# Kernel optimization log

Hardware: AMD Instinct MI355X
Metric: run time of the kernel (lower is better)

Reference implementation:

```python
import jax, jax.numpy as jnp
import numpy as np

KLD_SCALE = 10.0


def setup_inputs() -> dict:
    key = jax.random.key(0)
    k1, k2 = jax.random.split(key)
    B, C, H, W = 16, 64, 64, 64
    K = 1024
    inputs = jax.random.normal(k1, (B, C, H, W), dtype=jnp.float32)
    codebook = jax.random.normal(k2, (K, C), dtype=jnp.float32) * (1.0 / K)
    beta = jnp.float32(0.25)
    return {"inputs": inputs, "codebook": codebook, "beta": beta}


def reference(inputs, codebook, beta):
    # inputs: [B, C, H, W], codebook: [K, D] with D == C
    sg = jax.lax.stop_gradient
    x = jnp.transpose(inputs, (0, 2, 3, 1))          # [B, H, W, D]
    D = x.shape[-1]
    flat = x.reshape(-1, D)                           # [N, D]
    d = (jnp.sum(flat * flat, axis=1, keepdims=True)
         + jnp.sum(codebook * codebook, axis=1)
         - 2.0 * flat @ codebook.T)                   # [N, K]
    idx = jnp.argmin(d, axis=1)                       # [N]
    q = codebook[idx].reshape(x.shape)                # gather == one_hot @ codebook
    # training (non-EMA) loss: (beta*||q - sg(x)||^2 + ||sg(q) - x||^2) * kld_scale
    loss = beta * jnp.mean((q - sg(x)) ** 2)
    loss = (loss + jnp.mean((sg(q) - x) ** 2)) * KLD_SCALE
    # straight-through estimator
    q_st = x + sg(q - x)
    # perplexity from code usage histogram (== mean of one-hot rows)
    K = codebook.shape[0]
    counts = jnp.zeros((K,), dtype=flat.dtype).at[idx].add(1.0)
    e_mean = counts / flat.shape[0]
    perplexity = jnp.exp(-jnp.sum(e_mean * jnp.log(e_mean + 1e-10)))
    quantized = jnp.transpose(q_st, (0, 3, 1, 2))     # [B, C, H, W]
    return loss, quantized, perplexity
```

## Files before the change

kernel.cpp:

```cpp
#include <hip/hip_runtime.h>
#include <cfloat>

typedef __bf16 bf16x8 __attribute__((ext_vector_type(8)));
typedef float f32x16 __attribute__((ext_vector_type(16)));

namespace {
constexpr int kHW = 4096;
constexpr int kC = 64;
constexpr float kInvN = 1.0f / 65536.0f;


__global__ __launch_bounds__(256) void prep_kernel(
    const float* __restrict__ cb, uint4* __restrict__ frags,
    unsigned int* __restrict__ hist, float* __restrict__ lossacc) {
  const int c = blockIdx.x;
  const int t = threadIdx.x;
  const int lane = t & 63, wv = t >> 6;
  const int lo = lane & 31, hi = lane >> 5;
  const int code = c * 32 + lo;
  const int ks = wv;

  const float* row = cb + code * kC + ks * 16 + hi * 8;
  float4 v0 = *reinterpret_cast<const float4*>(row);
  float4 v1 = *reinterpret_cast<const float4*>(row + 4);
  float vv[8] = {v0.x, v0.y, v0.z, v0.w, v1.x, v1.y, v1.z, v1.w};
  bf16x8 fh, fl;
  #pragma unroll
  for (int e = 0; e < 8; ++e) {
    float v = -2.0f * vv[e];
    __bf16 h = (__bf16)v;
    fh[e] = h;
    fl[e] = (__bf16)(v - (float)h);
  }
  frags[(c * 9 + ks) * 64 + lane] = *reinterpret_cast<uint4*>(&fh);
  frags[(c * 9 + 4 + ks) * 64 + lane] = *reinterpret_cast<uint4*>(&fl);

  if (wv == 0) {
    bf16x8 fb;
    #pragma unroll
    for (int e = 0; e < 8; ++e) fb[e] = (__bf16)0.0f;
    if (hi == 0) {
      float s = 0.0f;
      #pragma unroll
      for (int d = 0; d < kC; d += 4) {
        float4 v = *reinterpret_cast<const float4*>(cb + code * kC + d);
        s = fmaf(v.x, v.x, fmaf(v.y, v.y, fmaf(v.z, v.z, fmaf(v.w, v.w, s))));
      }
      __bf16 h = (__bf16)s;
      fb[0] = h;
      fb[1] = (__bf16)(s - (float)h);
    }
    frags[(c * 9 + 8) * 64 + lane] = *reinterpret_cast<uint4*>(&fb);
  }
  if (t < 32) hist[c * 32 + t] = 0u;
  if (c == 0 && t == 0) lossacc[0] = 0.0f;
}

__global__ __launch_bounds__(256) void vq_argmin_kernel(
    const float* __restrict__ in, const bf16x8* __restrict__ frags,
    unsigned int* __restrict__ hist, unsigned int* __restrict__ idxOut) {
  __shared__ float sVal[4][32];
  __shared__ int sIdxW[4][32];
  const int t = threadIdx.x;
  const int lane = t & 63, wv = t >> 6;
  const int lo = lane & 31, hi = lane >> 5;
  const int sg2 = wv & 1, kh = wv >> 1;
  const int site = blockIdx.x * 64 + sg2 * 32 + lo;
  const int b = site >> 12, hw = site & 4095;
  const float* xp = in + b * (kC * kHW) + hw;

  bf16x8 Bh[4], Bl[4];
  #pragma unroll
  for (int ks = 0; ks < 4; ++ks) {
    #pragma unroll
    for (int e = 0; e < 8; ++e) {
      const int d = ks * 16 + hi * 8 + e;
      float v = xp[d * kHW];
      __bf16 h = (__bf16)v;
      Bh[ks][e] = h;
      Bl[ks][e] = (__bf16)(v - (float)h);
    }
  }
  bf16x8 ones;
  #pragma unroll
  for (int e = 0; e < 8; ++e) ones[e] = (__bf16)0.0f;
  if (hi == 0) { ones[0] = (__bf16)1.0f; ones[1] = (__bf16)1.0f; }
  f32x16 zero;
  #pragma unroll
  for (int r = 0; r < 16; ++r) zero[r] = 0.0f;

  float best[16];
  int bch[16];
  #pragma unroll
  for (int r = 0; r < 16; ++r) { best[r] = FLT_MAX; bch[r] = 0; }

  const bf16x8* fA = frags + lane;

  bf16x8 A0[9], A1[9];
  auto prefetch = [&](bf16x8(&F)[9], int c) {
    #pragma unroll
    for (int j = 0; j < 9; ++j) F[j] = fA[(c * 9 + j) * 64];
  };
  auto compute = [&](const bf16x8(&F)[9], int c) {
    f32x16 a = __builtin_amdgcn_mfma_f32_32x32x16_bf16(F[8], ones, zero, 0, 0, 0);
    #pragma unroll
    for (int ks = 0; ks < 4; ++ks)
      a = __builtin_amdgcn_mfma_f32_32x32x16_bf16(F[ks], Bh[ks], a, 0, 0, 0);
    #pragma unroll
    for (int ks = 0; ks < 4; ++ks)
      a = __builtin_amdgcn_mfma_f32_32x32x16_bf16(F[4 + ks], Bh[ks], a, 0, 0, 0);
    #pragma unroll
    for (int ks = 0; ks < 4; ++ks)
      a = __builtin_amdgcn_mfma_f32_32x32x16_bf16(F[ks], Bl[ks], a, 0, 0, 0);
    #pragma unroll
    for (int r = 0; r < 16; ++r) {
      bool p = a[r] < best[r];
      best[r] = p ? a[r] : best[r];
      bch[r] = p ? c : bch[r];
    }
  };

  const int c0 = kh * 16;
  prefetch(A0, c0);
  #pragma unroll 1
  for (int c = c0; c < c0 + 16; c += 2) {
    prefetch(A1, c + 1);
    compute(A0, c);
    if (c + 2 < c0 + 16) prefetch(A0, c + 2);
    compute(A1, c + 1);
  }

  float bv = best[0];
  int bidx = bch[0] * 32 + (hi << 2);
  #pragma unroll
  for (int r = 1; r < 16; ++r) {
    const int kloc = (r & 3) + 8 * (r >> 2) + (hi << 2);
    int idx = bch[r] * 32 + kloc;
    float v = best[r];
    if (v < bv || (v == bv && idx < bidx)) { bv = v; bidx = idx; }
  }
  float ov = __shfl_xor(bv, 32, 64);
  int oi = __shfl_xor(bidx, 32, 64);
  if (ov < bv || (ov == bv && oi < bidx)) { bv = ov; bidx = oi; }
  if (hi == 0) {
    sVal[wv][lo] = bv;
    sIdxW[wv][lo] = bidx;
  }
  __syncthreads();
  if (wv < 2 && hi == 0) {
    float v2 = sVal[wv + 2][lo];
    int i2 = sIdxW[wv + 2][lo];
    if (v2 < bv || (v2 == bv && i2 < bidx)) { bv = v2; bidx = i2; }
    idxOut[site] = (unsigned int)bidx;
    atomicAdd(&hist[bidx], 1u);
  }
}

__global__ __launch_bounds__(256) void epilogue_kernel(
    const float* __restrict__ in, const float* __restrict__ cb,
    const unsigned int* __restrict__ idx, float* __restrict__ lossacc,
    float* __restrict__ qout) {
  __shared__ float sRed[4];
  const int t = threadIdx.x;
  const int sg = t & 63, dg = t >> 6;
  const int siteBase = blockIdx.x * 256 + sg * 4;
  const int b = siteBase >> 12, hw = siteBase & 4095;
  const float* xb = in + b * (kC * kHW) + hw;
  float* ob = qout + b * (kC * kHW) + hw;
  uint4 cc = *reinterpret_cast<const uint4*>(idx + siteBase);
  const float* q0 = cb + cc.x * kC;
  const float* q1 = cb + cc.y * kC;
  const float* q2 = cb + cc.z * kC;
  const float* q3 = cb + cc.w * kC;
  float ls = 0.0f;
  #pragma unroll
  for (int j = 0; j < 16; ++j) {
    const int d = dg * 16 + j;
    float4 xv = *reinterpret_cast<const float4*>(xb + d * kHW);
    float d0 = q0[d] - xv.x;
    float d1 = q1[d] - xv.y;
    float d2 = q2[d] - xv.z;
    float d3 = q3[d] - xv.w;
    ls = fmaf(d0, d0, ls);
    ls = fmaf(d1, d1, ls);
    ls = fmaf(d2, d2, ls);
    ls = fmaf(d3, d3, ls);
    float* o = ob + d * kHW;
    o[0] = xv.x + d0;
    o[1] = xv.y + d1;
    o[2] = xv.z + d2;
    o[3] = xv.w + d3;
  }
  #pragma unroll
  for (int off = 32; off; off >>= 1) ls += __shfl_xor(ls, off, 64);
  if ((t & 63) == 0) sRed[t >> 6] = ls;
  __syncthreads();
  if (t == 0) {
    float s = (sRed[0] + sRed[1]) + (sRed[2] + sRed[3]);
    atomicAdd(lossacc, s);
  }
}

__global__ __launch_bounds__(1024) void finalize_kernel(
    const unsigned int* __restrict__ hist, const float* __restrict__ lossacc,
    const float* __restrict__ beta, float* __restrict__ out) {
  __shared__ float red[16];
  const int t = threadIdx.x;
  float e = (float)hist[t] * kInvN;
  float term = e * logf(e + 1e-10f);
  #pragma unroll
  for (int off = 32; off; off >>= 1) term += __shfl_xor(term, off, 64);
  if ((t & 63) == 0) red[t >> 6] = term;
  __syncthreads();
  if (t == 0) {
    float h = 0.0f;
    #pragma unroll
    for (int i = 0; i < 16; ++i) h += red[i];
    out[1 + 4194304] = expf(-h);
    out[0] = lossacc[0] * (1.0f + beta[0]) * 10.0f / 4194304.0f;
  }
}
}

extern "C" void kernel_launch(void* const* d_in, const int* in_sizes, int n_in,
                              void* d_out, int out_size, void* d_ws, size_t ws_size,
                              hipStream_t stream) {
  const float* inputs = (const float*)d_in[0];
  const float* cb = (const float*)d_in[1];
  const float* beta = (const float*)d_in[2];
  float* out = (float*)d_out;

  uint4* frags = (uint4*)d_ws;
  unsigned int* hist = (unsigned int*)((char*)d_ws + 294912);
  float* lossacc = (float*)((char*)d_ws + 299008);
  unsigned int* idx = (unsigned int*)((char*)d_ws + 299024);

  prep_kernel<<<32, 256, 0, stream>>>(cb, frags, hist, lossacc);
  vq_argmin_kernel<<<1024, 256, 0, stream>>>(inputs, (const bf16x8*)frags,
                                             hist, idx);
  epilogue_kernel<<<256, 256, 0, stream>>>(inputs, cb, idx, lossacc, out + 1);
  finalize_kernel<<<1, 1024, 0, stream>>>(hist, lossacc, beta, out);
}
```

Baseline: 121.2 us.

## Split codebook across four waves, each handling all 64 sites

Each wave now processes both 32-site groups of the block against one quarter of the codebook, instead of half the codebook for one site group. Every loaded codebook fragment feeds two independent MFMA chains, so each wave reads half as many fragment bytes per MFMA and has two accumulators to interleave and hide latency. The cost is roughly doubled register use for inputs, accumulators and best values, which may lower occupancy. The final reduction now merges four partial results per site in one wave.

After: 124.3 us. +2.5%, slower.

```diff
diff --git a/kernel.cpp b/kernel.cpp
--- a/kernel.cpp
+++ b/kernel.cpp
@@ -59,26 +59,31 @@
 __global__ __launch_bounds__(256) void vq_argmin_kernel(
     const float* __restrict__ in, const bf16x8* __restrict__ frags,
     unsigned int* __restrict__ hist, unsigned int* __restrict__ idxOut) {
-  __shared__ float sVal[4][32];
-  __shared__ int sIdxW[4][32];
+  __shared__ float sVal[4][64];
+  __shared__ int sIdxW[4][64];
   const int t = threadIdx.x;
   const int lane = t & 63, wv = t >> 6;
   const int lo = lane & 31, hi = lane >> 5;
-  const int sg2 = wv & 1, kh = wv >> 1;
-  const int site = blockIdx.x * 64 + sg2 * 32 + lo;
-  const int b = site >> 12, hw = site & 4095;
-  const float* xp = in + b * (kC * kHW) + hw;
-
-  bf16x8 Bh[4], Bl[4];
+  const int siteBase = blockIdx.x * 64;
+  const int b = siteBase >> 12;
+  const int hw0 = siteBase & 4095;
+  const float* xp0 = in + b * (kC * kHW) + hw0 + lo;
+  const float* xp1 = in + b * (kC * kHW) + hw0 + 32 + lo;
+
+  bf16x8 B0h[4], B0l[4], B1h[4], B1l[4];
   #pragma unroll
   for (int ks = 0; ks < 4; ++ks) {
     #pragma unroll
     for (int e = 0; e < 8; ++e) {
       const int d = ks * 16 + hi * 8 + e;
-      float v = xp[d * kHW];
-      __bf16 h = (__bf16)v;
-      Bh[ks][e] = h;
-      Bl[ks][e] = (__bf16)(v - (float)h);
+      float v0 = xp0[d * kHW];
+      __bf16 h0 = (__bf16)v0;
+      B0h[ks][e] = h0;
+      B0l[ks][e] = (__bf16)(v0 - (float)h0);
+      float v1 = xp1[d * kHW];
+      __bf16 h1 = (__bf16)v1;
+      B1h[ks][e] = h1;
+      B1l[ks][e] = (__bf16)(v1 - (float)h1);
     }
   }
   bf16x8 ones;
@@ -89,10 +94,13 @@
   #pragma unroll
   for (int r = 0; r < 16; ++r) zero[r] = 0.0f;
 
-  float best[16];
-  int bch[16];
-  #pragma unroll
-  for (int r = 0; r < 16; ++r) { best[r] = FLT_MAX; bch[r] = 0; }
+  float best0[16], best1[16];
+  int bch0[16], bch1[16];
+  #pragma unroll
+  for (int r = 0; r < 16; ++r) {
+    best0[r] = FLT_MAX; bch0[r] = 0;
+    best1[r] = FLT_MAX; bch1[r] = 0;
+  }
 
   const bf16x8* fA = frags + lane;
 
@@ -102,57 +110,81 @@
     for (int j = 0; j < 9; ++j) F[j] = fA[(c * 9 + j) * 64];
   };
   auto compute = [&](const bf16x8(&F)[9], int c) {
-    f32x16 a = __builtin_amdgcn_mfma_f32_32x32x16_bf16(F[8], ones, zero, 0, 0, 0);
-    #pragma unroll
-    for (int ks = 0; ks < 4; ++ks)
-      a = __builtin_amdgcn_mfma_f32_32x32x16_bf16(F[ks], Bh[ks], a, 0, 0, 0);
-    #pragma unroll
-    for (int ks = 0; ks < 4; ++ks)
-      a = __builtin_amdgcn_mfma_f32_32x32x16_bf16(F[4 + ks], Bh[ks], a, 0, 0, 0);
-    #pragma unroll
-    for (int ks = 0; ks < 4; ++ks)
-      a = __builtin_amdgcn_mfma_f32_32x32x16_bf16(F[ks], Bl[ks], a, 0, 0, 0);
+    f32x16 a0 = __builtin_amdgcn_mfma_f32_32x32x16_bf16(F[8], ones, zero, 0, 0, 0);
+    f32x16 a1 = __builtin_amdgcn_mfma_f32_32x32x16_bf16(F[8], ones, zero, 0, 0, 0);
+    #pragma unroll
+    for (int ks = 0; ks < 4; ++ks) {
+      a0 = __builtin_amdgcn_mfma_f32_32x32x16_bf16(F[ks], B0h[ks], a0, 0, 0, 0);
+      a1 = __builtin_amdgcn_mfma_f32_32x32x16_bf16(F[ks], B1h[ks], a1, 0, 0, 0);
+    }
+    #pragma unroll
+    for (int ks = 0; ks < 4; ++ks) {
+      a0 = __builtin_amdgcn_mfma_f32_32x32x16_bf16(F[4 + ks], B0h[ks], a0, 0, 0, 0);
+      a1 = __builtin_amdgcn_mfma_f32_32x32x16_bf16(F[4 + ks], B1h[ks], a1, 0, 0, 0);
+    }
+    #pragma unroll
+    for (int ks = 0; ks < 4; ++ks) {
+      a0 = __builtin_amdgcn_mfma_f32_32x32x16_bf16(F[ks], B0l[ks], a0, 0, 0, 0);
+      a1 = __builtin_amdgcn_mfma_f32_32x32x16_bf16(F[ks], B1l[ks], a1, 0, 0, 0);
+    }
     #pragma unroll
     for (int r = 0; r < 16; ++r) {
-      bool p = a[r] < best[r];
-      best[r] = p ? a[r] : best[r];
-      bch[r] = p ? c : bch[r];
+      bool p0 = a0[r] < best0[r];
+      best0[r] = p0 ? a0[r] : best0[r];
+      bch0[r] = p0 ? c : bch0[r];
+      bool p1 = a1[r] < best1[r];
+      best1[r] = p1 ? a1[r] : best1[r];
+      bch1[r] = p1 ? c : bch1[r];
     }
   };
 
-  const int c0 = kh * 16;
+  const int c0 = wv * 8;
   prefetch(A0, c0);
   #pragma unroll 1
-  for (int c = c0; c < c0 + 16; c += 2) {
+  for (int c = c0; c < c0 + 8; c += 2) {
     prefetch(A1, c + 1);
     compute(A0, c);
-    if (c + 2 < c0 + 16) prefetch(A0, c + 2);
+    if (c + 2 < c0 + 8) prefetch(A0, c + 2);
     compute(A1, c + 1);
   }
 
-  float bv = best[0];
-  int bidx = bch[0] * 32 + (hi << 2);
+  float bv0 = best0[0], bv1 = best1[0];
+  int bi0 = bch0[0] * 32 + (hi << 2);
+  int bi1 = bch1[0] * 32 + (hi << 2);
   #pragma unroll
   for (int r = 1; r < 16; ++r) {
     const int kloc = (r & 3) + 8 * (r >> 2) + (hi << 2);
-    int idx = bch[r] * 32 + kloc;
-    float v = best[r];
-    if (v < bv || (v == bv && idx < bidx)) { bv = v; bidx = idx; }
-  }
-  float ov = __shfl_xor(bv, 32, 64);
-  int oi = __shfl_xor(bidx, 32, 64);
-  if (ov < bv || (ov == bv && oi < bidx)) { bv = ov; bidx = oi; }
+    int i0 = bch0[r] * 32 + kloc;
+    float v0 = best0[r];
+    if (v0 < bv0 || (v0 == bv0 && i0 < bi0)) { bv0 = v0; bi0 = i0; }
+    int i1 = bch1[r] * 32 + kloc;
+    float v1 = best1[r];
+    if (v1 < bv1 || (v1 == bv1 && i1 < bi1)) { bv1 = v1; bi1 = i1; }
+  }
+  {
+    float ov = __shfl_xor(bv0, 32, 64);
+    int oi = __shfl_xor(bi0, 32, 64);
+    if (ov < bv0 || (ov == bv0 && oi < bi0)) { bv0 = ov; bi0 = oi; }
+    ov = __shfl_xor(bv1, 32, 64);
+    oi = __shfl_xor(bi1, 32, 64);
+    if (ov < bv1 || (ov == bv1 && oi < bi1)) { bv1 = ov; bi1 = oi; }
+  }
   if (hi == 0) {
-    sVal[wv][lo] = bv;
-    sIdxW[wv][lo] = bidx;
+    sVal[wv][lo] = bv0;       sIdxW[wv][lo] = bi0;
+    sVal[wv][32 + lo] = bv1;  sIdxW[wv][32 + lo] = bi1;
   }
   __syncthreads();
-  if (wv < 2 && hi == 0) {
-    float v2 = sVal[wv + 2][lo];
-    int i2 = sIdxW[wv + 2][lo];
-    if (v2 < bv || (v2 == bv && i2 < bidx)) { bv = v2; bidx = i2; }
-    idxOut[site] = (unsigned int)bidx;
-    atomicAdd(&hist[bidx], 1u);
+  if (wv == 0) {
+    float bb = sVal[0][lane];
+    int bi = sIdxW[0][lane];
+    #pragma unroll
+    for (int w2 = 1; w2 < 4; ++w2) {
+      float v2 = sVal[w2][lane];
+      int i2 = sIdxW[w2][lane];
+      if (v2 < bb || (v2 == bb && i2 < bi)) { bb = v2; bi = i2; }
+    }
+    idxOut[siteBase + lane] = (unsigned int)bi;
+    atomicAdd(&hist[bi], 1u);
   }
 }
 
```

## Stage input tile through LDS with vector loads and fully unroll codebook loop

Applied to the files above, without the earlier changes.

Each block now loads its 64x64 input tile into shared memory using coalesced float4 global loads, and waves build their bf16 hi/lo fragments from LDS. Before, each lane issued strided scalar global loads, and each input element was fetched twice, once by each codebook-half wave. The manual double-buffered prefetch of codebook fragments is replaced by a fully unrolled 16-iteration loop, leaving load scheduling to the compiler. This adds 16KB of LDS per block and a barrier, and the full unroll may raise register pressure and lower occupancy.

After: 138.6 us. 1.14x slower.

```diff
diff --git a/kernel.cpp b/kernel.cpp
--- a/kernel.cpp
+++ b/kernel.cpp
@@ -59,26 +59,40 @@
 __global__ __launch_bounds__(256) void vq_argmin_kernel(
     const float* __restrict__ in, const bf16x8* __restrict__ frags,
     unsigned int* __restrict__ hist, unsigned int* __restrict__ idxOut) {
+  __shared__ __align__(16) float sX[64][64];
   __shared__ float sVal[4][32];
   __shared__ int sIdxW[4][32];
   const int t = threadIdx.x;
   const int lane = t & 63, wv = t >> 6;
   const int lo = lane & 31, hi = lane >> 5;
-  const int sg2 = wv & 1, kh = wv >> 1;
-  const int site = blockIdx.x * 64 + sg2 * 32 + lo;
-  const int b = site >> 12, hw = site & 4095;
-  const float* xp = in + b * (kC * kHW) + hw;
+  const int g = wv & 1, h = wv >> 1;
+  const int siteBase = blockIdx.x * 64;
+  const int b = siteBase >> 12, hw0 = siteBase & 4095;
+  const float* xin = in + b * (kC * kHW) + hw0;
+
+  {
+    const int s4 = (t & 15) * 4;
+    const int d0 = t >> 4;
+    #pragma unroll
+    for (int i = 0; i < 4; ++i) {
+      const int d = d0 + i * 16;
+      *reinterpret_cast<float4*>(&sX[d][s4]) =
+          *reinterpret_cast<const float4*>(xin + d * kHW + s4);
+    }
+  }
+  __syncthreads();
 
   bf16x8 Bh[4], Bl[4];
+  const int col = g * 32 + lo;
   #pragma unroll
   for (int ks = 0; ks < 4; ++ks) {
     #pragma unroll
     for (int e = 0; e < 8; ++e) {
       const int d = ks * 16 + hi * 8 + e;
-      float v = xp[d * kHW];
-      __bf16 h = (__bf16)v;
-      Bh[ks][e] = h;
-      Bl[ks][e] = (__bf16)(v - (float)h);
+      float v = sX[d][col];
+      __bf16 hh = (__bf16)v;
+      Bh[ks][e] = hh;
+      Bl[ks][e] = (__bf16)(v - (float)hh);
     }
   }
   bf16x8 ones;
@@ -95,13 +109,14 @@
   for (int r = 0; r < 16; ++r) { best[r] = FLT_MAX; bch[r] = 0; }
 
   const bf16x8* fA = frags + lane;
-
-  bf16x8 A0[9], A1[9];
-  auto prefetch = [&](bf16x8(&F)[9], int c) {
+  const int c0 = h * 16;
+
+  #pragma unroll
+  for (int cc = 0; cc < 16; ++cc) {
+    const int c = c0 + cc;
+    bf16x8 F[9];
     #pragma unroll
     for (int j = 0; j < 9; ++j) F[j] = fA[(c * 9 + j) * 64];
-  };
-  auto compute = [&](const bf16x8(&F)[9], int c) {
     f32x16 a = __builtin_amdgcn_mfma_f32_32x32x16_bf16(F[8], ones, zero, 0, 0, 0);
     #pragma unroll
     for (int ks = 0; ks < 4; ++ks)
@@ -118,16 +133,6 @@
       best[r] = p ? a[r] : best[r];
       bch[r] = p ? c : bch[r];
     }
-  };
-
-  const int c0 = kh * 16;
-  prefetch(A0, c0);
-  #pragma unroll 1
-  for (int c = c0; c < c0 + 16; c += 2) {
-    prefetch(A1, c + 1);
-    compute(A0, c);
-    if (c + 2 < c0 + 16) prefetch(A0, c + 2);
-    compute(A1, c + 1);
   }
 
   float bv = best[0];
@@ -151,7 +156,7 @@
     float v2 = sVal[wv + 2][lo];
     int i2 = sIdxW[wv + 2][lo];
     if (v2 < bv || (v2 == bv && i2 < bidx)) { bv = v2; bidx = i2; }
-    idxOut[site] = (unsigned int)bidx;
+    idxOut[siteBase + g * 32 + lo] = (unsigned int)bidx;
     atomicAdd(&hist[bidx], 1u);
   }
 }
```

## Stage codebook fragments in LDS and give each wave all codes for its sites

Applied to the files above, without the earlier changes.

The argmin kernel now uses 512-thread blocks, each covering 256 sites. Each wave scans the full codebook for its own 32 sites, so the cross-wave LDS reduction goes away. Codebook fragments are copied into a 147KB LDS buffer in two halves with global_load_lds, instead of every wave reading them from global/L2. The MFMA chain is split into two independent accumulators to shorten dependency chains. Risks: the large LDS footprint allows only one block per CU, the 256-block grid is small, and the staging is serialized with no overlap between halves.

New measurement: 124.6 us. 2.8% more time.

```diff
diff --git a/kernel.cpp b/kernel.cpp
--- a/kernel.cpp
+++ b/kernel.cpp
@@ -8,6 +8,8 @@
 constexpr int kHW = 4096;
 constexpr int kC = 64;
 constexpr float kInvN = 1.0f / 65536.0f;
+constexpr int kChunkBytes = 9216;
+constexpr int kHalfBytes = 16 * kChunkBytes;
 
 
 __global__ __launch_bounds__(256) void prep_kernel(
@@ -56,18 +58,28 @@
   if (c == 0 && t == 0) lossacc[0] = 0.0f;
 }
 
-__global__ __launch_bounds__(256) void vq_argmin_kernel(
-    const float* __restrict__ in, const bf16x8* __restrict__ frags,
+__global__ __launch_bounds__(512) void vq_argmin_kernel(
+    const float* __restrict__ in, const char* __restrict__ fragsB,
     unsigned int* __restrict__ hist, unsigned int* __restrict__ idxOut) {
-  __shared__ float sVal[4][32];
-  __shared__ int sIdxW[4][32];
+  __shared__ __align__(16) char sF[kHalfBytes];
   const int t = threadIdx.x;
   const int lane = t & 63, wv = t >> 6;
   const int lo = lane & 31, hi = lane >> 5;
-  const int sg2 = wv & 1, kh = wv >> 1;
-  const int site = blockIdx.x * 64 + sg2 * 32 + lo;
+  const int site = blockIdx.x * 256 + wv * 32 + lo;
   const int b = site >> 12, hw = site & 4095;
   const float* xp = in + b * (kC * kHW) + hw;
+
+  auto stage = [&](int h) {
+    const char* g = fragsB + h * kHalfBytes;
+    #pragma unroll
+    for (int r = 0; r < 18; ++r) {
+      const int off = r * 8192 + wv * 1024 + lane * 16;
+      __builtin_amdgcn_global_load_lds((const uint32_t*)(g + off),
+                                       (uint32_t*)(sF + off), 16, 0, 0);
+    }
+  };
+
+  stage(0);
 
   bf16x8 Bh[4], Bl[4];
   #pragma unroll
@@ -76,9 +88,9 @@
     for (int e = 0; e < 8; ++e) {
       const int d = ks * 16 + hi * 8 + e;
       float v = xp[d * kHW];
-      __bf16 h = (__bf16)v;
-      Bh[ks][e] = h;
-      Bl[ks][e] = (__bf16)(v - (float)h);
+      __bf16 hh = (__bf16)v;
+      Bh[ks][e] = hh;
+      Bl[ks][e] = (__bf16)(v - (float)hh);
     }
   }
   bf16x8 ones;
@@ -94,41 +106,45 @@
   #pragma unroll
   for (int r = 0; r < 16; ++r) { best[r] = FLT_MAX; bch[r] = 0; }
 
-  const bf16x8* fA = frags + lane;
-
-  bf16x8 A0[9], A1[9];
-  auto prefetch = [&](bf16x8(&F)[9], int c) {
-    #pragma unroll
-    for (int j = 0; j < 9; ++j) F[j] = fA[(c * 9 + j) * 64];
+  auto scanHalf = [&](int gbase) {
+    #pragma unroll 2
+    for (int c = 0; c < 16; ++c) {
+      const char* lb = sF + c * kChunkBytes + lane * 16;
+      bf16x8 F[9];
+      #pragma unroll
+      for (int j = 0; j < 9; ++j)
+        F[j] = *reinterpret_cast<const bf16x8*>(lb + j * 1024);
+      f32x16 a1 = __builtin_amdgcn_mfma_f32_32x32x16_bf16(F[8], ones, zero, 0, 0, 0);
+      f32x16 a2 = zero;
+      #pragma unroll
+      for (int ks = 0; ks < 4; ++ks)
+        a1 = __builtin_amdgcn_mfma_f32_32x32x16_bf16(F[ks], Bh[ks], a1, 0, 0, 0);
+      #pragma unroll
+      for (int ks = 0; ks < 4; ++ks)
+        a2 = __builtin_amdgcn_mfma_f32_32x32x16_bf16(F[4 + ks], Bh[ks], a2, 0, 0, 0);
+      #pragma unroll
+      for (int ks = 0; ks < 4; ++ks)
+        a2 = __builtin_amdgcn_mfma_f32_32x32x16_bf16(F[ks], Bl[ks], a2, 0, 0, 0);
+      const int gc = gbase + c;
+      #pragma unroll
+      for (int r = 0; r < 16; ++r) {
+        float d = a1[r] + a2[r];
+        bool p = d < best[r];
+        best[r] = p ? d : best[r];
+        bch[r] = p ? gc : bch[r];
+      }
+    }
   };
-  auto compute = [&](const bf16x8(&F)[9], int c) {
-    f32x16 a = __builtin_amdgcn_mfma_f32_32x32x16_bf16(F[8], ones, zero, 0, 0, 0);
-    #pragma unroll
-    for (int ks = 0; ks < 4; ++ks)
-      a = __builtin_amdgcn_mfma_f32_32x32x16_bf16(F[ks], Bh[ks], a, 0, 0, 0);
-    #pragma unroll
-    for (int ks = 0; ks < 4; ++ks)
-      a = __builtin_amdgcn_mfma_f32_32x32x16_bf16(F[4 + ks], Bh[ks], a, 0, 0, 0);
-    #pragma unroll
-    for (int ks = 0; ks < 4; ++ks)
-      a = __builtin_amdgcn_mfma_f32_32x32x16_bf16(F[ks], Bl[ks], a, 0, 0, 0);
-    #pragma unroll
-    for (int r = 0; r < 16; ++r) {
-      bool p = a[r] < best[r];
-      best[r] = p ? a[r] : best[r];
-      bch[r] = p ? c : bch[r];
-    }
-  };
-
-  const int c0 = kh * 16;
-  prefetch(A0, c0);
-  #pragma unroll 1
-  for (int c = c0; c < c0 + 16; c += 2) {
-    prefetch(A1, c + 1);
-    compute(A0, c);
-    if (c + 2 < c0 + 16) prefetch(A0, c + 2);
-    compute(A1, c + 1);
-  }
+
+  asm volatile("s_waitcnt vmcnt(0)" ::: "memory");
+  __syncthreads();
+  scanHalf(0);
+
+  __syncthreads();
+  stage(1);
+  asm volatile("s_waitcnt vmcnt(0)" ::: "memory");
+  __syncthreads();
+  scanHalf(16);
 
   float bv = best[0];
   int bidx = bch[0] * 32 + (hi << 2);
@@ -143,14 +159,6 @@
   int oi = __shfl_xor(bidx, 32, 64);
   if (ov < bv || (ov == bv && oi < bidx)) { bv = ov; bidx = oi; }
   if (hi == 0) {
-    sVal[wv][lo] = bv;
-    sIdxW[wv][lo] = bidx;
-  }
-  __syncthreads();
-  if (wv < 2 && hi == 0) {
-    float v2 = sVal[wv + 2][lo];
-    int i2 = sIdxW[wv + 2][lo];
-    if (v2 < bv || (v2 == bv && i2 < bidx)) { bv = v2; bidx = i2; }
     idxOut[site] = (unsigned int)bidx;
     atomicAdd(&hist[bidx], 1u);
   }
@@ -236,8 +244,8 @@
   unsigned int* idx = (unsigned int*)((char*)d_ws + 299024);
 
   prep_kernel<<<32, 256, 0, stream>>>(cb, frags, hist, lossacc);
-  vq_argmin_kernel<<<1024, 256, 0, stream>>>(inputs, (const bf16x8*)frags,
-                                             hist, idx);
+  vq_argmin_kernel<<<256, 512, 0, stream>>>(inputs, (const char*)d_ws,
+                                            hist, idx);
   epilogue_kernel<<<256, 256, 0, stream>>>(inputs, cb, idx, lossacc, out + 1);
   finalize_kernel<<<1, 1024, 0, stream>>>(hist, lossacc, beta, out);
 }
```
